# Kernel tuning notes

Hardware: AMD Instinct MI355X
Metric: run time of the kernel (lower is better)

## Reference

```python
import jax, jax.numpy as jnp
import numpy as np

N = 50000
E = 800000
NUM_GRAPHS = 64

def gat_layer(x, W, att_src, att_dst, bias, src, dst, heads, out_ch, concat):
    n = x.shape[0]
    h = (x @ W).reshape(n, heads, out_ch)                      # [N,H,C]
    a_s = jnp.sum(h * att_src, axis=-1)                        # [N,H]
    a_d = jnp.sum(h * att_dst, axis=-1)                        # [N,H]
    e = jax.nn.leaky_relu(a_s[src] + a_d[dst], 0.2)            # [E,H]
    m = jax.ops.segment_max(e, dst, num_segments=n)            # segment softmax (self-loops guarantee non-empty)
    e = jnp.exp(e - m[dst])
    s = jax.ops.segment_sum(e, dst, num_segments=n)
    alpha = e / s[dst]                                         # [E,H]
    out = jax.ops.segment_sum(alpha[:, :, None] * h[src], dst, num_segments=n)  # [N,H,C]
    out = out.reshape(n, heads * out_ch) if concat else out.mean(axis=1)
    return out + bias

def setup_inputs() -> dict:
    key = jax.random.key(0)
    ks = jax.random.split(key, 20)
    inp = {}
    inp['x'] = jax.random.normal(ks[0], (N, 256), dtype=jnp.float32)
    inp['edge_index'] = jax.random.randint(ks[1], (2, E), 0, N, dtype=jnp.int64)
    inp['batch'] = jnp.sort(jax.random.randint(ks[2], (N,), 0, NUM_GRAPHS, dtype=jnp.int64))
    s = 0.05
    inp['W1'] = jax.random.normal(ks[3], (256, 256), dtype=jnp.float32) * s
    inp['att_src1'] = jax.random.normal(ks[4], (8, 32), dtype=jnp.float32) * s
    inp['att_dst1'] = jax.random.normal(ks[5], (8, 32), dtype=jnp.float32) * s
    inp['b1'] = jax.random.normal(ks[6], (256,), dtype=jnp.float32) * s
    inp['W2'] = jax.random.normal(ks[7], (256, 256), dtype=jnp.float32) * s
    inp['att_src2'] = jax.random.normal(ks[8], (8, 32), dtype=jnp.float32) * s
    inp['att_dst2'] = jax.random.normal(ks[9], (8, 32), dtype=jnp.float32) * s
    inp['b2'] = jax.random.normal(ks[10], (256,), dtype=jnp.float32) * s
    inp['W3'] = jax.random.normal(ks[11], (256, 32), dtype=jnp.float32) * s
    inp['att_src3'] = jax.random.normal(ks[12], (1, 32), dtype=jnp.float32) * s
    inp['att_dst3'] = jax.random.normal(ks[13], (1, 32), dtype=jnp.float32) * s
    inp['b3'] = jax.random.normal(ks[14], (32,), dtype=jnp.float32) * s
    inp['linW'] = jax.random.normal(ks[15], (32, 1), dtype=jnp.float32) * s
    inp['linb'] = jax.random.normal(ks[16], (1,), dtype=jnp.float32) * s
    return inp

def reference(x, edge_index, batch, W1, att_src1, att_dst1, b1, W2, att_src2, att_dst2, b2,
              W3, att_src3, att_dst3, b3, linW, linb):
    # add self loops (PyG add_self_loops=True)
    loop = jnp.arange(N, dtype=edge_index.dtype)
    src = jnp.concatenate([edge_index[0], loop])
    dst = jnp.concatenate([edge_index[1], loop])
    # eval mode: dropout is identity
    h = gat_layer(x, W1, att_src1, att_dst1, b1, src, dst, 8, 32, True)
    h = jax.nn.elu(h)
    h = gat_layer(h, W2, att_src2, att_dst2, b2, src, dst, 8, 32, True)
    h = jax.nn.elu(h)
    h = gat_layer(h, W3, att_src3, att_dst3, b3, src, dst, 1, 32, False)
    # global mean pool over all nodes (topic_mask defaults to all True)
    sums = jax.ops.segment_sum(h, batch, num_segments=NUM_GRAPHS)
    cnts = jax.ops.segment_sum(jnp.ones((N,), h.dtype), batch, num_segments=NUM_GRAPHS)
    pooled = sums / jnp.maximum(cnts, 1.0)[:, None]
    out = pooled @ linW + linb                                  # [G,1]
    return out.squeeze(-1)                                      # num_classes==2
```

## Files before the change

kernel.cpp:

```cpp
#include <hip/hip_runtime.h>
#include <hip/hip_fp8.h>
#include <math.h>


typedef __attribute__((ext_vector_type(8))) __bf16 bf16x8;
typedef __attribute__((ext_vector_type(4))) __bf16 bf16x4;
typedef __attribute__((ext_vector_type(4))) float f32x4;
typedef __attribute__((ext_vector_type(2))) float f32x2;

#define SCAN_CH 4

__device__ inline unsigned char f32_to_fp8(float f) {
  __hip_fp8_e4m3 v(f);
  return (unsigned char)v.__x;
}
__device__ inline float fp8_to_f32(unsigned char u) {
  __hip_fp8_e4m3 v;
  v.__x = (__hip_fp8_storage_t)u;
  return (float)v;
}

__device__ inline void fma_fp8x4(f32x4& acc, float w, unsigned int packed) {
#if defined(__has_builtin) && __has_builtin(__builtin_amdgcn_cvt_pk_f32_fp8)
  f32x2 lo = __builtin_amdgcn_cvt_pk_f32_fp8((int)packed, false);
  f32x2 hi = __builtin_amdgcn_cvt_pk_f32_fp8((int)packed, true);
  acc[0] += w * lo[0];
  acc[1] += w * lo[1];
  acc[2] += w * hi[0];
  acc[3] += w * hi[1];
#else
  acc[0] += w * fp8_to_f32((unsigned char)(packed & 0xff));
  acc[1] += w * fp8_to_f32((unsigned char)((packed >> 8) & 0xff));
  acc[2] += w * fp8_to_f32((unsigned char)((packed >> 16) & 0xff));
  acc[3] += w * fp8_to_f32((unsigned char)(packed >> 24));
#endif
}

__global__ __launch_bounds__(256) void k_init_deg(int* deg, int N) {
  int n = blockIdx.x * 256 + threadIdx.x;
  if (n < N) deg[n] = 1;
}

__global__ __launch_bounds__(256) void k_count_deg(const int* __restrict__ ei,
                                                   int E, int* deg) {
  int e = blockIdx.x * 256 + threadIdx.x;
  if (e < E) atomicAdd(&deg[ei[E + e]], 1);
}

__global__ __launch_bounds__(256) void k_scan_partial(const int* __restrict__ deg,
                                                      int* __restrict__ blockSums,
                                                      int N) {
  __shared__ int sh[256];
  int t = threadIdx.x, b = blockIdx.x;
  int base = (b * 256 + t) * SCAN_CH;
  int s = 0;
#pragma unroll
  for (int j = 0; j < SCAN_CH; j++) {
    int idx = base + j;
    if (idx < N) s += deg[idx];
  }
  sh[t] = s;
  __syncthreads();
  for (int off = 128; off > 0; off >>= 1) {
    if (t < off) sh[t] += sh[t + off];
    __syncthreads();
  }
  if (t == 0) blockSums[b] = sh[0];
}

__global__ __launch_bounds__(256) void k_scan_blocksums(
    const int* __restrict__ blockSums, int* __restrict__ blockOffs,
    int* __restrict__ rowptr, int nb, int N) {
  __shared__ int sh[256];
  int t = threadIdx.x;
  int v = (t < nb) ? blockSums[t] : 0;
  sh[t] = v;
  __syncthreads();
  for (int off = 1; off < 256; off <<= 1) {
    int u = (t >= off) ? sh[t - off] : 0;
    __syncthreads();
    sh[t] += u;
    __syncthreads();
  }
  if (t < nb) blockOffs[t] = sh[t] - v;
  if (t == nb - 1) rowptr[N] = sh[t];
}

__global__ __launch_bounds__(256) void k_scan_final(const int* __restrict__ deg,
                                                    const int* __restrict__ blockOffs,
                                                    int* __restrict__ rowptr,
                                                    int* __restrict__ cursor, int N) {
  __shared__ int sh[256];
  int t = threadIdx.x, b = blockIdx.x;
  int base = (b * 256 + t) * SCAN_CH;
  int vals[SCAN_CH];
  int s = 0;
#pragma unroll
  for (int j = 0; j < SCAN_CH; j++) {
    int idx = base + j;
    vals[j] = (idx < N) ? deg[idx] : 0;
    s += vals[j];
  }
  sh[t] = s;
  __syncthreads();
  for (int off = 1; off < 256; off <<= 1) {
    int u = (t >= off) ? sh[t - off] : 0;
    __syncthreads();
    sh[t] += u;
    __syncthreads();
  }
  int run = blockOffs[b] + sh[t] - s;
#pragma unroll
  for (int j = 0; j < SCAN_CH; j++) {
    int idx = base + j;
    if (idx < N) {
      rowptr[idx] = run;
      cursor[idx] = run;
      run += vals[j];
    }
  }
}

__global__ __launch_bounds__(256) void k_scatter2(const int* __restrict__ ei,
                                                  int E, int N, int* cursor,
                                                  int2* __restrict__ col2,
                                                  int chunkSz) {
  int stripe = blockIdx.x & 7;
  int chunk = blockIdx.x >> 3;
  int lo = (int)(((long long)N * stripe) >> 3);
  int hi = (int)(((long long)N * (stripe + 1)) >> 3);
  int base = chunk * chunkSz;
  int end = base + chunkSz;
  int total = E + N;
  if (end > total) end = total;
  for (int i = base + threadIdx.x; i < end; i += 256) {
    int d = (i < E) ? ei[E + i] : (i - E);
    if (d < lo || d >= hi) continue;
    int s = (i < E) ? ei[i] : d;
    int pos = atomicAdd(&cursor[d], 1);
    col2[pos] = make_int2(s, d);
  }
}

__global__ __launch_bounds__(256) void k_split(const float* __restrict__ in,
                                               __bf16* __restrict__ oh,
                                               __bf16* __restrict__ ol, int n4) {
  int i = blockIdx.x * 256 + threadIdx.x;
  if (i >= n4) return;
  float4 v = ((const float4*)in)[i];
  bf16x4 h, l;
  h[0] = (__bf16)v.x; l[0] = (__bf16)(v.x - (float)h[0]);
  h[1] = (__bf16)v.y; l[1] = (__bf16)(v.y - (float)h[1]);
  h[2] = (__bf16)v.z; l[2] = (__bf16)(v.z - (float)h[2]);
  h[3] = (__bf16)v.w; l[3] = (__bf16)(v.w - (float)h[3]);
  ((bf16x4*)oh)[i] = h;
  ((bf16x4*)ol)[i] = l;
}

__global__ __launch_bounds__(256) void k_wprep(const float* __restrict__ W,
                                               __bf16* __restrict__ WTh,
                                               int K, int Nc) {
  int i = blockIdx.x * 256 + threadIdx.x;
  if (i >= K * Nc) return;
  int n = i / K, k = i - n * K;
  WTh[i] = (__bf16)W[k * Nc + n];
}

__global__ __launch_bounds__(256) void k_gemm_lds(
    const __bf16* __restrict__ Ah, const __bf16* __restrict__ Al,
    const __bf16* __restrict__ BTh,
    __bf16* __restrict__ Ch, unsigned char* __restrict__ Cf8, int M, int K) {
  constexpr int NcFull = 256;
  __shared__ __bf16 sAh[2][2048];
  __shared__ __bf16 sAl[2][2048];
  int tid = threadIdx.x;
  int lane = tid & 63, wave = tid >> 6;
  int quad = lane >> 4, l16 = lane & 15;
  int m0 = blockIdx.x * 64;
  int col0 = wave * 64;
  int sr = tid >> 2, skq = tid & 3;
  int slot8 = (((sr >> 4) * 4 + skq) * 16 + (sr & 15)) * 8;
  int arow = min(m0 + sr, M - 1);
  const __bf16* agh = Ah + (size_t)arow * K + skq * 8;
  const __bf16* agl = Al + (size_t)arow * K + skq * 8;
  const __bf16* brh = BTh + (size_t)(col0 + l16) * K + quad * 8;
  f32x4 acc[4][4];
#pragma unroll
  for (int mt = 0; mt < 4; mt++)
#pragma unroll
    for (int t = 0; t < 4; t++) acc[mt][t] = (f32x4){0.f, 0.f, 0.f, 0.f};
  *(bf16x8*)(sAh[0] + slot8) = *(const bf16x8*)agh;
  *(bf16x8*)(sAl[0] + slot8) = *(const bf16x8*)agl;
  __syncthreads();
  int buf = 0;
  for (int k0 = 0; k0 < K; k0 += 32, buf ^= 1) {
    bool more = (k0 + 32 < K);
    bf16x8 gh, gl;
    if (more) {
      gh = *(const bf16x8*)(agh + k0 + 32);
      gl = *(const bf16x8*)(agl + k0 + 32);
    }
    bf16x8 b_h[4];
#pragma unroll
    for (int t = 0; t < 4; t++)
      b_h[t] = *(const bf16x8*)(brh + (size_t)t * 16 * K + k0);
    const __bf16* rh = sAh[buf];
    const __bf16* rl = sAl[buf];
    bf16x8 a_h[4], a_l[4];
#pragma unroll
    for (int mt = 0; mt < 4; mt++) {
      int fi = ((mt * 4 + quad) * 16 + l16) * 8;
      a_h[mt] = *(const bf16x8*)(rh + fi);
      a_l[mt] = *(const bf16x8*)(rl + fi);
    }
#pragma unroll
    for (int t = 0; t < 4; t++) {
#pragma unroll
      for (int mt = 0; mt < 4; mt++) {
        acc[mt][t] = __builtin_amdgcn_mfma_f32_16x16x32_bf16(a_h[mt], b_h[t], acc[mt][t], 0, 0, 0);
        acc[mt][t] = __builtin_amdgcn_mfma_f32_16x16x32_bf16(a_l[mt], b_h[t], acc[mt][t], 0, 0, 0);
      }
    }
    if (more) {
      *(bf16x8*)(sAh[buf ^ 1] + slot8) = gh;
      *(bf16x8*)(sAl[buf ^ 1] + slot8) = gl;
    }
    __syncthreads();
  }
#pragma unroll
  for (int mt = 0; mt < 4; mt++) {
#pragma unroll
    for (int t = 0; t < 4; t++) {
#pragma unroll
      for (int r = 0; r < 4; r++) {
        int m = m0 + mt * 16 + quad * 4 + r;
        if (m < M) {
          size_t o = (size_t)m * NcFull + col0 + t * 16 + l16;
          Ch[o] = (__bf16)acc[mt][t][r];
          Cf8[o] = f32_to_fp8(acc[mt][t][r]);
        }
      }
    }
  }
}

template <int NT, int MT>
__global__ __launch_bounds__(256) void k_gemm_split(
    const __bf16* __restrict__ Ah, const __bf16* __restrict__ Al,
    const __bf16* __restrict__ BTh,
    __bf16* __restrict__ Ch, int M, int K, int NcFull) {
  int lane = threadIdx.x & 63;
  int wave = threadIdx.x >> 6;
  int quad = lane >> 4;
  int l16 = lane & 15;
  int m0 = blockIdx.y * (64 * MT) + wave * (16 * MT);
  int col0 = blockIdx.x * (NT * 16);
  const __bf16* arh[MT];
  const __bf16* arl[MT];
#pragma unroll
  for (int mt = 0; mt < MT; mt++) {
    int am = min(m0 + mt * 16 + l16, M - 1);
    arh[mt] = Ah + (size_t)am * K + quad * 8;
    arl[mt] = Al + (size_t)am * K + quad * 8;
  }
  const __bf16* brh = BTh + (size_t)(col0 + l16) * K + quad * 8;
  f32x4 acc[MT][NT];
#pragma unroll
  for (int mt = 0; mt < MT; mt++)
#pragma unroll
    for (int t = 0; t < NT; t++) acc[mt][t] = (f32x4){0.f, 0.f, 0.f, 0.f};
  for (int k0 = 0; k0 < K; k0 += 32) {
    bf16x8 a_h[MT], a_l[MT], b_h[NT];
#pragma unroll
    for (int mt = 0; mt < MT; mt++) {
      a_h[mt] = *(const bf16x8*)(arh[mt] + k0);
      a_l[mt] = *(const bf16x8*)(arl[mt] + k0);
    }
#pragma unroll
    for (int t = 0; t < NT; t++)
      b_h[t] = *(const bf16x8*)(brh + (size_t)t * 16 * K + k0);
#pragma unroll
    for (int t = 0; t < NT; t++) {
#pragma unroll
      for (int mt = 0; mt < MT; mt++) {
        acc[mt][t] = __builtin_amdgcn_mfma_f32_16x16x32_bf16(a_h[mt], b_h[t], acc[mt][t], 0, 0, 0);
        acc[mt][t] = __builtin_amdgcn_mfma_f32_16x16x32_bf16(a_l[mt], b_h[t], acc[mt][t], 0, 0, 0);
      }
    }
  }
#pragma unroll
  for (int mt = 0; mt < MT; mt++) {
#pragma unroll
    for (int t = 0; t < NT; t++) {
#pragma unroll
      for (int r = 0; r < 4; r++) {
        int m = m0 + mt * 16 + quad * 4 + r;
        if (m < M)
          Ch[(size_t)m * NcFull + col0 + t * 16 + l16] = (__bf16)acc[mt][t][r];
      }
    }
  }
}

__global__ __launch_bounds__(256) void k_att(const __bf16* __restrict__ Hh,
                                             const float* __restrict__ attS,
                                             const float* __restrict__ attD,
                                             float* __restrict__ aS,
                                             float* __restrict__ aD, int NH, int H) {
  int idx = blockIdx.x * 256 + threadIdx.x;
  if (idx >= NH) return;
  int h = idx % H;
  const bf16x8* hv = (const bf16x8*)(Hh + (size_t)idx * 32);
  const float* sv = attS + h * 32;
  const float* dv = attD + h * 32;
  float ss = 0.f, dd = 0.f;
#pragma unroll
  for (int k = 0; k < 4; k++) {
    bf16x8 a = hv[k];
#pragma unroll
    for (int j = 0; j < 8; j++) {
      float v = (float)a[j];
      ss += v * sv[k * 8 + j];
      dd += v * dv[k * 8 + j];
    }
  }
  aS[idx] = ss;
  aD[idx] = dd;
}

__global__ __launch_bounds__(256) void k_edge_alpha8(
    const float* __restrict__ aS, const float* __restrict__ aD,
    const int2* __restrict__ col2,
    __bf16* __restrict__ ealpha, int M) {
  int e = blockIdx.x * 256 + threadIdx.x;
  if (e >= M) return;
  int2 sd = col2[e];
  const float* ap = aS + (size_t)sd.x * 8;
  const float* dp = aD + (size_t)sd.y * 8;
  bf16x8 ev;
#pragma unroll
  for (int h = 0; h < 8; h++) {
    float x = ap[h] + dp[h];
    x = (x > 0.f) ? x : 0.2f * x;
    ev[h] = (__bf16)__expf(x);
  }
  *(bf16x8*)(ealpha + (size_t)e * 8) = ev;
}

__global__ __launch_bounds__(256) void k_edge_alpha1(
    const float* __restrict__ aS, const float* __restrict__ aD,
    const int2* __restrict__ col2,
    __bf16* __restrict__ ealpha, int M) {
  int e = blockIdx.x * 256 + threadIdx.x;
  if (e >= M) return;
  int2 sd = col2[e];
  float x = aS[sd.x] + aD[sd.y];
  x = (x > 0.f) ? x : 0.2f * x;
  ealpha[e] = (__bf16)__expf(x);
}

__global__ __launch_bounds__(256) void k_gat_agg8(
    const unsigned char* __restrict__ Hf8, const int* __restrict__ rowptr,
    const int2* __restrict__ col2, const __bf16* __restrict__ ealpha,
    const float* __restrict__ bias, __bf16* __restrict__ outh,
    __bf16* __restrict__ outl, int N) {
  int wid = (blockIdx.x * blockDim.x + threadIdx.x) >> 6;
  int lane = threadIdx.x & 63;
  if (wid >= N) return;
  int n = wid;
  int row0 = rowptr[n];
  int deg = rowptr[n + 1] - row0;
  int head = lane >> 3;

  f32x4 acc = (f32x4){0.f, 0.f, 0.f, 0.f};
  float den = 0.f;
  const __bf16* ea = ealpha;
  int i = 0;
  for (; i + 3 < deg; i += 4) {
    int sl = row0 + i;
    int s0 = col2[sl + 0].x;
    int s1 = col2[sl + 1].x;
    int s2 = col2[sl + 2].x;
    int s3 = col2[sl + 3].x;
    float w0 = (float)ea[(size_t)(sl + 0) * 8 + head];
    float w1 = (float)ea[(size_t)(sl + 1) * 8 + head];
    float w2 = (float)ea[(size_t)(sl + 2) * 8 + head];
    float w3 = (float)ea[(size_t)(sl + 3) * 8 + head];
    unsigned int p0 = *(const unsigned int*)(Hf8 + (size_t)s0 * 256 + lane * 4);
    unsigned int p1 = *(const unsigned int*)(Hf8 + (size_t)s1 * 256 + lane * 4);
    unsigned int p2 = *(const unsigned int*)(Hf8 + (size_t)s2 * 256 + lane * 4);
    unsigned int p3 = *(const unsigned int*)(Hf8 + (size_t)s3 * 256 + lane * 4);
    den += w0 + w1 + w2 + w3;
    fma_fp8x4(acc, w0, p0);
    fma_fp8x4(acc, w1, p1);
    fma_fp8x4(acc, w2, p2);
    fma_fp8x4(acc, w3, p3);
  }
  for (; i < deg; i++) {
    int sl = row0 + i;
    int s0 = col2[sl].x;
    float w0 = (float)ea[(size_t)sl * 8 + head];
    unsigned int p0 = *(const unsigned int*)(Hf8 + (size_t)s0 * 256 + lane * 4);
    den += w0;
    fma_fp8x4(acc, w0, p0);
  }
  float rsv = 1.f / den;
  float4 bv = *(const float4*)(bias + lane * 4);
  bf16x4 hb, lb;
#pragma unroll
  for (int j = 0; j < 4; j++) {
    float v = acc[j] * rsv + ((const float*)&bv)[j];
    v = (v > 0.f) ? v : (__expf(v) - 1.f);
    hb[j] = (__bf16)v;
    lb[j] = (__bf16)(v - (float)hb[j]);
  }
  *(bf16x4*)(outh + (size_t)n * 256 + lane * 4) = hb;
  *(bf16x4*)(outl + (size_t)n * 256 + lane * 4) = lb;
}

__global__ __launch_bounds__(256) void k_gat_agg1(
    const __bf16* __restrict__ Hh, const int* __restrict__ rowptr,
    const int2* __restrict__ col2, const __bf16* __restrict__ ealpha,
    const float* __restrict__ bias, float* __restrict__ out, int N) {
  int wid = (blockIdx.x * blockDim.x + threadIdx.x) >> 6;
  int lane = threadIdx.x & 63;
  if (wid >= N) return;
  int n = wid;
  int row0 = rowptr[n];
  int deg = rowptr[n + 1] - row0;
  int eo = lane >> 3;
  int cl = lane & 7;
  f32x4 acc = (f32x4){0.f, 0.f, 0.f, 0.f};
  float den = 0.f;
  for (int i = eo; i < deg; i += 8) {
    int slot = row0 + i;
    int src = col2[slot].x;
    float w = (float)ealpha[slot];
    den += w;
    bf16x4 hv = *(const bf16x4*)(Hh + (size_t)src * 32 + cl * 4);
#pragma unroll
    for (int j = 0; j < 4; j++) acc[j] += w * (float)hv[j];
  }
#pragma unroll
  for (int off = 8; off < 64; off <<= 1) {
#pragma unroll
    for (int j = 0; j < 4; j++) acc[j] += __shfl_xor(acc[j], off, 64);
    den += __shfl_xor(den, off, 64);
  }
  if (eo == 0) {
    float rsv = 1.f / den;
#pragma unroll
    for (int j = 0; j < 4; j++)
      out[(size_t)n * 32 + cl * 4 + j] = acc[j] * rsv + bias[cl * 4 + j];
  }
}

__global__ __launch_bounds__(256) void k_pool_final(
    const float* __restrict__ h, const int* __restrict__ batch,
    const float* __restrict__ linW, const float* __restrict__ linb,
    float* __restrict__ out, int N) {
  __shared__ float sh[256];
  int g = blockIdx.x;
  int tid = threadIdx.x;
  int grp = tid >> 5, c = tid & 31;
  int lo = 0, hi = N;
  while (lo < hi) { int mid = (lo + hi) >> 1; if (batch[mid] < g) lo = mid + 1; else hi = mid; }
  int start = lo;
  hi = N;
  while (lo < hi) { int mid = (lo + hi) >> 1; if (batch[mid] < g + 1) lo = mid + 1; else hi = mid; }
  int end = lo;
  float acc = 0.f;
  for (int n = start + grp; n < end; n += 8) acc += h[(size_t)n * 32 + c];
  sh[tid] = acc;
  __syncthreads();
  if (tid < 32) {
    float s = 0.f;
#pragma unroll
    for (int j = 0; j < 8; j++) s += sh[j * 32 + tid];
    float v = s * linW[tid];
#pragma unroll
    for (int off = 16; off > 0; off >>= 1) v += __shfl_xor(v, off, 64);
    if (tid == 0) {
      float cnt = (float)(end - start);
      out[g] = v / fmaxf(cnt, 1.f) + linb[0];
    }
  }
}

extern "C" void kernel_launch(void* const* d_in, const int* in_sizes, int n_in,
                              void* d_out, int out_size, void* d_ws, size_t ws_size,
                              hipStream_t stream) {
  const float* x = (const float*)d_in[0];
  const int* ei = (const int*)d_in[1];
  const int* batch = (const int*)d_in[2];
  const float* W1 = (const float*)d_in[3];
  const float* as1 = (const float*)d_in[4];
  const float* ad1 = (const float*)d_in[5];
  const float* b1 = (const float*)d_in[6];
  const float* W2 = (const float*)d_in[7];
  const float* as2 = (const float*)d_in[8];
  const float* ad2 = (const float*)d_in[9];
  const float* b2 = (const float*)d_in[10];
  const float* W3 = (const float*)d_in[11];
  const float* as3 = (const float*)d_in[12];
  const float* ad3 = (const float*)d_in[13];
  const float* b3 = (const float*)d_in[14];
  const float* linW = (const float*)d_in[15];
  const float* linb = (const float*)d_in[16];

  const int N = in_sizes[0] / 256;
  const int E = in_sizes[1] / 2;
  const int NUM_GRAPHS = 64;
  float* out = (float*)d_out;

  char* ws = (char*)d_ws;
  size_t off = 0;
  auto alloc = [&](size_t bytes) -> void* {
    void* p = ws + off;
    off += (bytes + 255) & ~(size_t)255;
    return p;
  };
  __bf16* Hh = (__bf16*)alloc((size_t)N * 256 * 2);
  unsigned char* Hf8 = (unsigned char*)alloc((size_t)N * 256);
  __bf16* Ah = (__bf16*)alloc((size_t)N * 256 * 2);
  __bf16* Al = (__bf16*)alloc((size_t)N * 256 * 2);
  __bf16* ealpha = (__bf16*)alloc((size_t)(E + N) * 8 * 2);
  float* aS = (float*)alloc((size_t)N * 8 * 4);
  float* aD = (float*)alloc((size_t)N * 8 * 4);
  int* deg = (int*)alloc((size_t)N * 4);
  int* rowptr = (int*)alloc((size_t)(N + 1) * 4);
  int* cursor = (int*)alloc((size_t)(N + 1) * 4);
  int2* col2 = (int2*)alloc((size_t)(E + N) * 8);
  int* blockSums = (int*)alloc(256 * 4);
  int* blockOffs = (int*)alloc(256 * 4);
  __bf16* WT1h = (__bf16*)alloc(256 * 256 * 2);
  __bf16* WT2h = (__bf16*)alloc(256 * 256 * 2);
  __bf16* WT3h = (__bf16*)alloc(32 * 256 * 2);
  float* h3agg = (float*)Ah;

  k_split<<<(N * 64 + 255) / 256, 256, 0, stream>>>(x, Ah, Al, N * 64);
  k_wprep<<<(256 * 256 + 255) / 256, 256, 0, stream>>>(W1, WT1h, 256, 256);
  k_wprep<<<(256 * 256 + 255) / 256, 256, 0, stream>>>(W2, WT2h, 256, 256);
  k_wprep<<<(256 * 32 + 255) / 256, 256, 0, stream>>>(W3, WT3h, 256, 32);
  k_init_deg<<<(N + 255) / 256, 256, 0, stream>>>(deg, N);
  k_count_deg<<<(E + 255) / 256, 256, 0, stream>>>(ei, E, deg);
  const int nb = (N + 256 * SCAN_CH - 1) / (256 * SCAN_CH);
  k_scan_partial<<<nb, 256, 0, stream>>>(deg, blockSums, N);
  k_scan_blocksums<<<1, 256, 0, stream>>>(blockSums, blockOffs, rowptr, nb, N);
  k_scan_final<<<nb, 256, 0, stream>>>(deg, blockOffs, rowptr, cursor, N);
  {
    const int totalItems = E + N;
    const int nch = 256;
    const int chunkSz = (totalItems + nch - 1) / nch;
    k_scatter2<<<8 * nch, 256, 0, stream>>>(ei, E, N, cursor, col2, chunkSz);
  }

  const int aggBlocks = (N + 3) / 4;
  const int gemmBlocks = (N + 63) / 64;
  const int M = E + N;
  const int edgeBlocks = (M + 255) / 256;
  dim3 g3(1, (N + 63) / 64);

  k_gemm_lds<<<gemmBlocks, 256, 0, stream>>>(Ah, Al, WT1h, Hh, Hf8, N, 256);
  k_att<<<(N * 8 + 255) / 256, 256, 0, stream>>>(Hh, as1, ad1, aS, aD, N * 8, 8);
  k_edge_alpha8<<<edgeBlocks, 256, 0, stream>>>(aS, aD, col2, ealpha, M);
  k_gat_agg8<<<aggBlocks, 256, 0, stream>>>(Hf8, rowptr, col2, ealpha, b1,
                                            Ah, Al, N);
  k_gemm_lds<<<gemmBlocks, 256, 0, stream>>>(Ah, Al, WT2h, Hh, Hf8, N, 256);
  k_att<<<(N * 8 + 255) / 256, 256, 0, stream>>>(Hh, as2, ad2, aS, aD, N * 8, 8);
  k_edge_alpha8<<<edgeBlocks, 256, 0, stream>>>(aS, aD, col2, ealpha, M);
  k_gat_agg8<<<aggBlocks, 256, 0, stream>>>(Hf8, rowptr, col2, ealpha, b2,
                                            Ah, Al, N);
  k_gemm_split<2, 1><<<g3, 256, 0, stream>>>(Ah, Al, WT3h, Hh, N, 256, 32);
  k_att<<<(N + 255) / 256, 256, 0, stream>>>(Hh, as3, ad3, aS, aD, N, 1);
  k_edge_alpha1<<<edgeBlocks, 256, 0, stream>>>(aS, aD, col2, ealpha, M);
  k_gat_agg1<<<aggBlocks, 256, 0, stream>>>(Hh, rowptr, col2, ealpha, b3,
                                            h3agg, N);
  k_pool_final<<<NUM_GRAPHS, 256, 0, stream>>>(h3agg, batch, linW, linb, out, N);
}
```

Before: 506.4 us.

## Partition fp8 features and edge weights into column quarters for cache-local aggregation

The GEMM now writes its fp8 output as four 64-column planes, one per wave column slice, and edge attention weights are stored as four planes of head pairs. The aggregation kernel launches separate blocks per quarter, interleaved so that all blocks working on a quarter touch a table a quarter the size, improving L2 hit rates on random neighbor gathers. Each wave handles four edges in parallel with a shuffle reduction at the end. A separate source-index array is added so the gathers read 4-byte indices instead of int2 pairs. The cost is extra index writes during the scatter and four times as many rowptr, index and weight reads across quarters.

```diff
diff --git a/kernel.cpp b/kernel.cpp
--- a/kernel.cpp
+++ b/kernel.cpp
@@ -5,6 +5,7 @@
 
 typedef __attribute__((ext_vector_type(8))) __bf16 bf16x8;
 typedef __attribute__((ext_vector_type(4))) __bf16 bf16x4;
+typedef __attribute__((ext_vector_type(2))) __bf16 bf16x2;
 typedef __attribute__((ext_vector_type(4))) float f32x4;
 typedef __attribute__((ext_vector_type(2))) float f32x2;
 
@@ -124,6 +125,7 @@
 __global__ __launch_bounds__(256) void k_scatter2(const int* __restrict__ ei,
                                                   int E, int N, int* cursor,
                                                   int2* __restrict__ col2,
+                                                  int* __restrict__ col_s,
                                                   int chunkSz) {
   int stripe = blockIdx.x & 7;
   int chunk = blockIdx.x >> 3;
@@ -139,6 +141,7 @@
     int s = (i < E) ? ei[i] : d;
     int pos = atomicAdd(&cursor[d], 1);
     col2[pos] = make_int2(s, d);
+    col_s[pos] = s;
   }
 }
 
@@ -235,9 +238,9 @@
       for (int r = 0; r < 4; r++) {
         int m = m0 + mt * 16 + quad * 4 + r;
         if (m < M) {
-          size_t o = (size_t)m * NcFull + col0 + t * 16 + l16;
-          Ch[o] = (__bf16)acc[mt][t][r];
-          Cf8[o] = f32_to_fp8(acc[mt][t][r]);
+          int colq = t * 16 + l16;
+          Ch[(size_t)m * NcFull + col0 + colq] = (__bf16)acc[mt][t][r];
+          Cf8[((size_t)wave * M + m) * 64 + colq] = f32_to_fp8(acc[mt][t][r]);
         }
       }
     }
@@ -331,20 +334,26 @@
 __global__ __launch_bounds__(256) void k_edge_alpha8(
     const float* __restrict__ aS, const float* __restrict__ aD,
     const int2* __restrict__ col2,
-    __bf16* __restrict__ ealpha, int M) {
+    __bf16* __restrict__ eaq, int M) {
   int e = blockIdx.x * 256 + threadIdx.x;
   if (e >= M) return;
   int2 sd = col2[e];
   const float* ap = aS + (size_t)sd.x * 8;
   const float* dp = aD + (size_t)sd.y * 8;
-  bf16x8 ev;
+  float ev[8];
 #pragma unroll
   for (int h = 0; h < 8; h++) {
     float x = ap[h] + dp[h];
     x = (x > 0.f) ? x : 0.2f * x;
-    ev[h] = (__bf16)__expf(x);
-  }
-  *(bf16x8*)(ealpha + (size_t)e * 8) = ev;
+    ev[h] = __expf(x);
+  }
+#pragma unroll
+  for (int q = 0; q < 4; q++) {
+    bf16x2 pr;
+    pr[0] = (__bf16)ev[2 * q];
+    pr[1] = (__bf16)ev[2 * q + 1];
+    *(bf16x2*)(eaq + ((size_t)q * M + e) * 2) = pr;
+  }
 }
 
 __global__ __launch_bounds__(256) void k_edge_alpha1(
@@ -359,68 +368,66 @@
   ealpha[e] = (__bf16)__expf(x);
 }
 
-__global__ __launch_bounds__(256) void k_gat_agg8(
-    const unsigned char* __restrict__ Hf8, const int* __restrict__ rowptr,
-    const int2* __restrict__ col2, const __bf16* __restrict__ ealpha,
+__global__ __launch_bounds__(256) void k_gat_agg8q(
+    const unsigned char* __restrict__ Hf8q, const int* __restrict__ rowptr,
+    const int* __restrict__ col_s, const __bf16* __restrict__ eaq,
     const float* __restrict__ bias, __bf16* __restrict__ outh,
-    __bf16* __restrict__ outl, int N) {
-  int wid = (blockIdx.x * blockDim.x + threadIdx.x) >> 6;
+    __bf16* __restrict__ outl, int N, int Mslots) {
+  int x = blockIdx.x & 7;
+  int q = x >> 1;
+  int chunk = (blockIdx.x >> 3) * 2 + (x & 1);
+  int wave = threadIdx.x >> 6;
+  int node = chunk * 4 + wave;
+  if (node >= N) return;
   int lane = threadIdx.x & 63;
-  if (wid >= N) return;
-  int n = wid;
-  int row0 = rowptr[n];
-  int deg = rowptr[n + 1] - row0;
-  int head = lane >> 3;
-
+  int g = lane >> 4;
+  int l = lane & 15;
+  int hh = l >> 3;
+  int row0 = rowptr[node];
+  int deg = rowptr[node + 1] - row0;
+  const unsigned char* tab = Hf8q + (size_t)q * ((size_t)N * 64);
+  const __bf16* ea = eaq + (size_t)q * ((size_t)Mslots * 2);
   f32x4 acc = (f32x4){0.f, 0.f, 0.f, 0.f};
   float den = 0.f;
-  const __bf16* ea = ealpha;
-  int i = 0;
-  for (; i + 3 < deg; i += 4) {
-    int sl = row0 + i;
-    int s0 = col2[sl + 0].x;
-    int s1 = col2[sl + 1].x;
-    int s2 = col2[sl + 2].x;
-    int s3 = col2[sl + 3].x;
-    float w0 = (float)ea[(size_t)(sl + 0) * 8 + head];
-    float w1 = (float)ea[(size_t)(sl + 1) * 8 + head];
-    float w2 = (float)ea[(size_t)(sl + 2) * 8 + head];
-    float w3 = (float)ea[(size_t)(sl + 3) * 8 + head];
-    unsigned int p0 = *(const unsigned int*)(Hf8 + (size_t)s0 * 256 + lane * 4);
-    unsigned int p1 = *(const unsigned int*)(Hf8 + (size_t)s1 * 256 + lane * 4);
-    unsigned int p2 = *(const unsigned int*)(Hf8 + (size_t)s2 * 256 + lane * 4);
-    unsigned int p3 = *(const unsigned int*)(Hf8 + (size_t)s3 * 256 + lane * 4);
-    den += w0 + w1 + w2 + w3;
+  for (int i = 0; i < deg; i += 8) {
+    int e0 = i + g, e1 = i + 4 + g;
+    int sl0 = row0 + min(e0, deg - 1);
+    int sl1 = row0 + min(e1, deg - 1);
+    int s0 = col_s[sl0];
+    int s1 = col_s[sl1];
+    float w0 = (e0 < deg) ? (float)ea[(size_t)sl0 * 2 + hh] : 0.f;
+    float w1 = (e1 < deg) ? (float)ea[(size_t)sl1 * 2 + hh] : 0.f;
+    unsigned int p0 = *(const unsigned int*)(tab + (size_t)s0 * 64 + l * 4);
+    unsigned int p1 = *(const unsigned int*)(tab + (size_t)s1 * 64 + l * 4);
+    den += w0 + w1;
     fma_fp8x4(acc, w0, p0);
     fma_fp8x4(acc, w1, p1);
-    fma_fp8x4(acc, w2, p2);
-    fma_fp8x4(acc, w3, p3);
-  }
-  for (; i < deg; i++) {
-    int sl = row0 + i;
-    int s0 = col2[sl].x;
-    float w0 = (float)ea[(size_t)sl * 8 + head];
-    unsigned int p0 = *(const unsigned int*)(Hf8 + (size_t)s0 * 256 + lane * 4);
-    den += w0;
-    fma_fp8x4(acc, w0, p0);
-  }
-  float rsv = 1.f / den;
-  float4 bv = *(const float4*)(bias + lane * 4);
-  bf16x4 hb, lb;
-#pragma unroll
-  for (int j = 0; j < 4; j++) {
-    float v = acc[j] * rsv + ((const float*)&bv)[j];
-    v = (v > 0.f) ? v : (__expf(v) - 1.f);
-    hb[j] = (__bf16)v;
-    lb[j] = (__bf16)(v - (float)hb[j]);
-  }
-  *(bf16x4*)(outh + (size_t)n * 256 + lane * 4) = hb;
-  *(bf16x4*)(outl + (size_t)n * 256 + lane * 4) = lb;
+  }
+#pragma unroll
+  for (int off = 16; off < 64; off <<= 1) {
+#pragma unroll
+    for (int j = 0; j < 4; j++) acc[j] += __shfl_xor(acc[j], off, 64);
+    den += __shfl_xor(den, off, 64);
+  }
+  if (g == 0) {
+    float rsv = 1.f / den;
+    float4 bv = *(const float4*)(bias + q * 64 + l * 4);
+    bf16x4 hb, lb;
+#pragma unroll
+    for (int j = 0; j < 4; j++) {
+      float v = acc[j] * rsv + ((const float*)&bv)[j];
+      v = (v > 0.f) ? v : (__expf(v) - 1.f);
+      hb[j] = (__bf16)v;
+      lb[j] = (__bf16)(v - (float)hb[j]);
+    }
+    *(bf16x4*)(outh + (size_t)node * 256 + q * 64 + l * 4) = hb;
+    *(bf16x4*)(outl + (size_t)node * 256 + q * 64 + l * 4) = lb;
+  }
 }
 
 __global__ __launch_bounds__(256) void k_gat_agg1(
     const __bf16* __restrict__ Hh, const int* __restrict__ rowptr,
-    const int2* __restrict__ col2, const __bf16* __restrict__ ealpha,
+    const int* __restrict__ col_s, const __bf16* __restrict__ ealpha,
     const float* __restrict__ bias, float* __restrict__ out, int N) {
   int wid = (blockIdx.x * blockDim.x + threadIdx.x) >> 6;
   int lane = threadIdx.x & 63;
@@ -434,7 +441,7 @@
   float den = 0.f;
   for (int i = eo; i < deg; i += 8) {
     int slot = row0 + i;
-    int src = col2[slot].x;
+    int src = col_s[slot];
     float w = (float)ealpha[slot];
     den += w;
     bf16x4 hv = *(const bf16x4*)(Hh + (size_t)src * 32 + cl * 4);
@@ -531,6 +538,7 @@
   int* rowptr = (int*)alloc((size_t)(N + 1) * 4);
   int* cursor = (int*)alloc((size_t)(N + 1) * 4);
   int2* col2 = (int2*)alloc((size_t)(E + N) * 8);
+  int* col_s = (int*)alloc((size_t)(E + N) * 4);
   int* blockSums = (int*)alloc(256 * 4);
   int* blockOffs = (int*)alloc(256 * 4);
   __bf16* WT1h = (__bf16*)alloc(256 * 256 * 2);
@@ -552,10 +560,12 @@
     const int totalItems = E + N;
     const int nch = 256;
     const int chunkSz = (totalItems + nch - 1) / nch;
-    k_scatter2<<<8 * nch, 256, 0, stream>>>(ei, E, N, cursor, col2, chunkSz);
+    k_scatter2<<<8 * nch, 256, 0, stream>>>(ei, E, N, cursor, col2, col_s, chunkSz);
   }
 
   const int aggBlocks = (N + 3) / 4;
+  const int nodeChunks = (N + 3) / 4;
+  const int agg8qGrid = 8 * ((nodeChunks + 1) / 2);
   const int gemmBlocks = (N + 63) / 64;
   const int M = E + N;
   const int edgeBlocks = (M + 255) / 256;
@@ -564,17 +574,17 @@
   k_gemm_lds<<<gemmBlocks, 256, 0, stream>>>(Ah, Al, WT1h, Hh, Hf8, N, 256);
   k_att<<<(N * 8 + 255) / 256, 256, 0, stream>>>(Hh, as1, ad1, aS, aD, N * 8, 8);
   k_edge_alpha8<<<edgeBlocks, 256, 0, stream>>>(aS, aD, col2, ealpha, M);
-  k_gat_agg8<<<aggBlocks, 256, 0, stream>>>(Hf8, rowptr, col2, ealpha, b1,
-                                            Ah, Al, N);
+  k_gat_agg8q<<<agg8qGrid, 256, 0, stream>>>(Hf8, rowptr, col_s, ealpha, b1,
+                                             Ah, Al, N, M);
   k_gemm_lds<<<gemmBlocks, 256, 0, stream>>>(Ah, Al, WT2h, Hh, Hf8, N, 256);
   k_att<<<(N * 8 + 255) / 256, 256, 0, stream>>>(Hh, as2, ad2, aS, aD, N * 8, 8);
   k_edge_alpha8<<<edgeBlocks, 256, 0, stream>>>(aS, aD, col2, ealpha, M);
-  k_gat_agg8<<<aggBlocks, 256, 0, stream>>>(Hf8, rowptr, col2, ealpha, b2,
-                                            Ah, Al, N);
+  k_gat_agg8q<<<agg8qGrid, 256, 0, stream>>>(Hf8, rowptr, col_s, ealpha, b2,
+                                             Ah, Al, N, M);
   k_gemm_split<2, 1><<<g3, 256, 0, stream>>>(Ah, Al, WT3h, Hh, N, 256, 32);
   k_att<<<(N + 255) / 256, 256, 0, stream>>>(Hh, as3, ad3, aS, aD, N, 1);
   k_edge_alpha1<<<edgeBlocks, 256, 0, stream>>>(aS, aD, col2, ealpha, M);
-  k_gat_agg1<<<aggBlocks, 256, 0, stream>>>(Hh, rowptr, col2, ealpha, b3,
+  k_gat_agg1<<<aggBlocks, 256, 0, stream>>>(Hh, rowptr, col_s, ealpha, b3,
                                             h3agg, N);
   k_pool_final<<<NUM_GRAPHS, 256, 0, stream>>>(h3agg, batch, linW, linb, out, N);
 }
```

Result: slower. 616.7 us (+21.8%).

## Drop bf16 hi/lo split of activations and use packed source index array

Applied to the files above, without the earlier changes.

Activations are no longer split into high and low bf16 halves, so every GEMM runs a single MFMA per tile instead of two, and the split/low-part stores and loads are removed. The scatter also writes a separate dense int array of source indices, which the aggregation kernels read instead of strided int2 pairs. The cost is lower GEMM input precision (plain bf16 activations), which could push results past the tolerance, plus one extra index array written during CSR build.

```diff
diff --git a/kernel.cpp b/kernel.cpp
--- a/kernel.cpp
+++ b/kernel.cpp
@@ -124,6 +124,7 @@
 __global__ __launch_bounds__(256) void k_scatter2(const int* __restrict__ ei,
                                                   int E, int N, int* cursor,
                                                   int2* __restrict__ col2,
+                                                  int* __restrict__ col_s,
                                                   int chunkSz) {
   int stripe = blockIdx.x & 7;
   int chunk = blockIdx.x >> 3;
@@ -139,22 +140,21 @@
     int s = (i < E) ? ei[i] : d;
     int pos = atomicAdd(&cursor[d], 1);
     col2[pos] = make_int2(s, d);
-  }
-}
-
-__global__ __launch_bounds__(256) void k_split(const float* __restrict__ in,
-                                               __bf16* __restrict__ oh,
-                                               __bf16* __restrict__ ol, int n4) {
+    col_s[pos] = s;
+  }
+}
+
+__global__ __launch_bounds__(256) void k_cast(const float* __restrict__ in,
+                                              __bf16* __restrict__ oh, int n4) {
   int i = blockIdx.x * 256 + threadIdx.x;
   if (i >= n4) return;
   float4 v = ((const float4*)in)[i];
-  bf16x4 h, l;
-  h[0] = (__bf16)v.x; l[0] = (__bf16)(v.x - (float)h[0]);
-  h[1] = (__bf16)v.y; l[1] = (__bf16)(v.y - (float)h[1]);
-  h[2] = (__bf16)v.z; l[2] = (__bf16)(v.z - (float)h[2]);
-  h[3] = (__bf16)v.w; l[3] = (__bf16)(v.w - (float)h[3]);
+  bf16x4 h;
+  h[0] = (__bf16)v.x;
+  h[1] = (__bf16)v.y;
+  h[2] = (__bf16)v.z;
+  h[3] = (__bf16)v.w;
   ((bf16x4*)oh)[i] = h;
-  ((bf16x4*)ol)[i] = l;
 }
 
 __global__ __launch_bounds__(256) void k_wprep(const float* __restrict__ W,
@@ -167,12 +167,10 @@
 }
 
 __global__ __launch_bounds__(256) void k_gemm_lds(
-    const __bf16* __restrict__ Ah, const __bf16* __restrict__ Al,
-    const __bf16* __restrict__ BTh,
+    const __bf16* __restrict__ Ah, const __bf16* __restrict__ BTh,
     __bf16* __restrict__ Ch, unsigned char* __restrict__ Cf8, int M, int K) {
   constexpr int NcFull = 256;
   __shared__ __bf16 sAh[2][2048];
-  __shared__ __bf16 sAl[2][2048];
   int tid = threadIdx.x;
   int lane = tid & 63, wave = tid >> 6;
   int quad = lane >> 4, l16 = lane & 15;
@@ -182,7 +180,6 @@
   int slot8 = (((sr >> 4) * 4 + skq) * 16 + (sr & 15)) * 8;
   int arow = min(m0 + sr, M - 1);
   const __bf16* agh = Ah + (size_t)arow * K + skq * 8;
-  const __bf16* agl = Al + (size_t)arow * K + skq * 8;
   const __bf16* brh = BTh + (size_t)(col0 + l16) * K + quad * 8;
   f32x4 acc[4][4];
 #pragma unroll
@@ -190,40 +187,34 @@
 #pragma unroll
     for (int t = 0; t < 4; t++) acc[mt][t] = (f32x4){0.f, 0.f, 0.f, 0.f};
   *(bf16x8*)(sAh[0] + slot8) = *(const bf16x8*)agh;
-  *(bf16x8*)(sAl[0] + slot8) = *(const bf16x8*)agl;
   __syncthreads();
   int buf = 0;
   for (int k0 = 0; k0 < K; k0 += 32, buf ^= 1) {
     bool more = (k0 + 32 < K);
-    bf16x8 gh, gl;
+    bf16x8 gh;
     if (more) {
       gh = *(const bf16x8*)(agh + k0 + 32);
-      gl = *(const bf16x8*)(agl + k0 + 32);
     }
     bf16x8 b_h[4];
 #pragma unroll
     for (int t = 0; t < 4; t++)
       b_h[t] = *(const bf16x8*)(brh + (size_t)t * 16 * K + k0);
     const __bf16* rh = sAh[buf];
-    const __bf16* rl = sAl[buf];
-    bf16x8 a_h[4], a_l[4];
+    bf16x8 a_h[4];
 #pragma unroll
     for (int mt = 0; mt < 4; mt++) {
       int fi = ((mt * 4 + quad) * 16 + l16) * 8;
       a_h[mt] = *(const bf16x8*)(rh + fi);
-      a_l[mt] = *(const bf16x8*)(rl + fi);
     }
 #pragma unroll
     for (int t = 0; t < 4; t++) {
 #pragma unroll
       for (int mt = 0; mt < 4; mt++) {
         acc[mt][t] = __builtin_amdgcn_mfma_f32_16x16x32_bf16(a_h[mt], b_h[t], acc[mt][t], 0, 0, 0);
-        acc[mt][t] = __builtin_amdgcn_mfma_f32_16x16x32_bf16(a_l[mt], b_h[t], acc[mt][t], 0, 0, 0);
       }
     }
     if (more) {
       *(bf16x8*)(sAh[buf ^ 1] + slot8) = gh;
-      *(bf16x8*)(sAl[buf ^ 1] + slot8) = gl;
     }
     __syncthreads();
   }
@@ -246,8 +237,7 @@
 
 template <int NT, int MT>
 __global__ __launch_bounds__(256) void k_gemm_split(
-    const __bf16* __restrict__ Ah, const __bf16* __restrict__ Al,
-    const __bf16* __restrict__ BTh,
+    const __bf16* __restrict__ Ah, const __bf16* __restrict__ BTh,
     __bf16* __restrict__ Ch, int M, int K, int NcFull) {
   int lane = threadIdx.x & 63;
   int wave = threadIdx.x >> 6;
@@ -256,12 +246,10 @@
   int m0 = blockIdx.y * (64 * MT) + wave * (16 * MT);
   int col0 = blockIdx.x * (NT * 16);
   const __bf16* arh[MT];
-  const __bf16* arl[MT];
 #pragma unroll
   for (int mt = 0; mt < MT; mt++) {
     int am = min(m0 + mt * 16 + l16, M - 1);
     arh[mt] = Ah + (size_t)am * K + quad * 8;
-    arl[mt] = Al + (size_t)am * K + quad * 8;
   }
   const __bf16* brh = BTh + (size_t)(col0 + l16) * K + quad * 8;
   f32x4 acc[MT][NT];
@@ -270,11 +258,10 @@
 #pragma unroll
     for (int t = 0; t < NT; t++) acc[mt][t] = (f32x4){0.f, 0.f, 0.f, 0.f};
   for (int k0 = 0; k0 < K; k0 += 32) {
-    bf16x8 a_h[MT], a_l[MT], b_h[NT];
+    bf16x8 a_h[MT], b_h[NT];
 #pragma unroll
     for (int mt = 0; mt < MT; mt++) {
       a_h[mt] = *(const bf16x8*)(arh[mt] + k0);
-      a_l[mt] = *(const bf16x8*)(arl[mt] + k0);
     }
 #pragma unroll
     for (int t = 0; t < NT; t++)
@@ -284,7 +271,6 @@
 #pragma unroll
       for (int mt = 0; mt < MT; mt++) {
         acc[mt][t] = __builtin_amdgcn_mfma_f32_16x16x32_bf16(a_h[mt], b_h[t], acc[mt][t], 0, 0, 0);
-        acc[mt][t] = __builtin_amdgcn_mfma_f32_16x16x32_bf16(a_l[mt], b_h[t], acc[mt][t], 0, 0, 0);
       }
     }
   }
@@ -361,9 +347,8 @@
 
 __global__ __launch_bounds__(256) void k_gat_agg8(
     const unsigned char* __restrict__ Hf8, const int* __restrict__ rowptr,
-    const int2* __restrict__ col2, const __bf16* __restrict__ ealpha,
-    const float* __restrict__ bias, __bf16* __restrict__ outh,
-    __bf16* __restrict__ outl, int N) {
+    const int* __restrict__ col_s, const __bf16* __restrict__ ealpha,
+    const float* __restrict__ bias, __bf16* __restrict__ outh, int N) {
   int wid = (blockIdx.x * blockDim.x + threadIdx.x) >> 6;
   int lane = threadIdx.x & 63;
   if (wid >= N) return;
@@ -378,10 +363,10 @@
   int i = 0;
   for (; i + 3 < deg; i += 4) {
     int sl = row0 + i;
-    int s0 = col2[sl + 0].x;
-    int s1 = col2[sl + 1].x;
-    int s2 = col2[sl + 2].x;
-    int s3 = col2[sl + 3].x;
+    int s0 = col_s[sl + 0];
+    int s1 = col_s[sl + 1];
+    int s2 = col_s[sl + 2];
+    int s3 = col_s[sl + 3];
     float w0 = (float)ea[(size_t)(sl + 0) * 8 + head];
     float w1 = (float)ea[(size_t)(sl + 1) * 8 + head];
     float w2 = (float)ea[(size_t)(sl + 2) * 8 + head];
@@ -398,7 +383,7 @@
   }
   for (; i < deg; i++) {
     int sl = row0 + i;
-    int s0 = col2[sl].x;
+    int s0 = col_s[sl];
     float w0 = (float)ea[(size_t)sl * 8 + head];
     unsigned int p0 = *(const unsigned int*)(Hf8 + (size_t)s0 * 256 + lane * 4);
     den += w0;
@@ -406,21 +391,19 @@
   }
   float rsv = 1.f / den;
   float4 bv = *(const float4*)(bias + lane * 4);
-  bf16x4 hb, lb;
+  bf16x4 hb;
 #pragma unroll
   for (int j = 0; j < 4; j++) {
     float v = acc[j] * rsv + ((const float*)&bv)[j];
     v = (v > 0.f) ? v : (__expf(v) - 1.f);
     hb[j] = (__bf16)v;
-    lb[j] = (__bf16)(v - (float)hb[j]);
   }
   *(bf16x4*)(outh + (size_t)n * 256 + lane * 4) = hb;
-  *(bf16x4*)(outl + (size_t)n * 256 + lane * 4) = lb;
 }
 
 __global__ __launch_bounds__(256) void k_gat_agg1(
     const __bf16* __restrict__ Hh, const int* __restrict__ rowptr,
-    const int2* __restrict__ col2, const __bf16* __restrict__ ealpha,
+    const int* __restrict__ col_s, const __bf16* __restrict__ ealpha,
     const float* __restrict__ bias, float* __restrict__ out, int N) {
   int wid = (blockIdx.x * blockDim.x + threadIdx.x) >> 6;
   int lane = threadIdx.x & 63;
@@ -434,7 +417,7 @@
   float den = 0.f;
   for (int i = eo; i < deg; i += 8) {
     int slot = row0 + i;
-    int src = col2[slot].x;
+    int src = col_s[slot];
     float w = (float)ealpha[slot];
     den += w;
     bf16x4 hv = *(const bf16x4*)(Hh + (size_t)src * 32 + cl * 4);
@@ -523,7 +506,6 @@
   __bf16* Hh = (__bf16*)alloc((size_t)N * 256 * 2);
   unsigned char* Hf8 = (unsigned char*)alloc((size_t)N * 256);
   __bf16* Ah = (__bf16*)alloc((size_t)N * 256 * 2);
-  __bf16* Al = (__bf16*)alloc((size_t)N * 256 * 2);
   __bf16* ealpha = (__bf16*)alloc((size_t)(E + N) * 8 * 2);
   float* aS = (float*)alloc((size_t)N * 8 * 4);
   float* aD = (float*)alloc((size_t)N * 8 * 4);
@@ -531,6 +513,7 @@
   int* rowptr = (int*)alloc((size_t)(N + 1) * 4);
   int* cursor = (int*)alloc((size_t)(N + 1) * 4);
   int2* col2 = (int2*)alloc((size_t)(E + N) * 8);
+  int* col_s = (int*)alloc((size_t)(E + N) * 4);
   int* blockSums = (int*)alloc(256 * 4);
   int* blockOffs = (int*)alloc(256 * 4);
   __bf16* WT1h = (__bf16*)alloc(256 * 256 * 2);
@@ -538,7 +521,7 @@
   __bf16* WT3h = (__bf16*)alloc(32 * 256 * 2);
   float* h3agg = (float*)Ah;
 
-  k_split<<<(N * 64 + 255) / 256, 256, 0, stream>>>(x, Ah, Al, N * 64);
+  k_cast<<<(N * 64 + 255) / 256, 256, 0, stream>>>(x, Ah, N * 64);
   k_wprep<<<(256 * 256 + 255) / 256, 256, 0, stream>>>(W1, WT1h, 256, 256);
   k_wprep<<<(256 * 256 + 255) / 256, 256, 0, stream>>>(W2, WT2h, 256, 256);
   k_wprep<<<(256 * 32 + 255) / 256, 256, 0, stream>>>(W3, WT3h, 256, 32);
@@ -552,7 +535,7 @@
     const int totalItems = E + N;
     const int nch = 256;
     const int chunkSz = (totalItems + nch - 1) / nch;
-    k_scatter2<<<8 * nch, 256, 0, stream>>>(ei, E, N, cursor, col2, chunkSz);
+    k_scatter2<<<8 * nch, 256, 0, stream>>>(ei, E, N, cursor, col2, col_s, chunkSz);
   }
 
   const int aggBlocks = (N + 3) / 4;
@@ -561,20 +544,20 @@
   const int edgeBlocks = (M + 255) / 256;
   dim3 g3(1, (N + 63) / 64);
 
-  k_gemm_lds<<<gemmBlocks, 256, 0, stream>>>(Ah, Al, WT1h, Hh, Hf8, N, 256);
+  k_gemm_lds<<<gemmBlocks, 256, 0, stream>>>(Ah, WT1h, Hh, Hf8, N, 256);
   k_att<<<(N * 8 + 255) / 256, 256, 0, stream>>>(Hh, as1, ad1, aS, aD, N * 8, 8);
   k_edge_alpha8<<<edgeBlocks, 256, 0, stream>>>(aS, aD, col2, ealpha, M);
-  k_gat_agg8<<<aggBlocks, 256, 0, stream>>>(Hf8, rowptr, col2, ealpha, b1,
-                                            Ah, Al, N);
-  k_gemm_lds<<<gemmBlocks, 256, 0, stream>>>(Ah, Al, WT2h, Hh, Hf8, N, 256);
+  k_gat_agg8<<<aggBlocks, 256, 0, stream>>>(Hf8, rowptr, col_s, ealpha, b1,
+                                            Ah, N);
+  k_gemm_lds<<<gemmBlocks, 256, 0, stream>>>(Ah, WT2h, Hh, Hf8, N, 256);
   k_att<<<(N * 8 + 255) / 256, 256, 0, stream>>>(Hh, as2, ad2, aS, aD, N * 8, 8);
   k_edge_alpha8<<<edgeBlocks, 256, 0, stream>>>(aS, aD, col2, ealpha, M);
-  k_gat_agg8<<<aggBlocks, 256, 0, stream>>>(Hf8, rowptr, col2, ealpha, b2,
-                                            Ah, Al, N);
-  k_gemm_split<2, 1><<<g3, 256, 0, stream>>>(Ah, Al, WT3h, Hh, N, 256, 32);
+  k_gat_agg8<<<aggBlocks, 256, 0, stream>>>(Hf8, rowptr, col_s, ealpha, b2,
+                                            Ah, N);
+  k_gemm_split<2, 1><<<g3, 256, 0, stream>>>(Ah, WT3h, Hh, N, 256, 32);
   k_att<<<(N + 255) / 256, 256, 0, stream>>>(Hh, as3, ad3, aS, aD, N, 1);
   k_edge_alpha1<<<edgeBlocks, 256, 0, stream>>>(aS, aD, col2, ealpha, M);
-  k_gat_agg1<<<aggBlocks, 256, 0, stream>>>(Hh, rowptr, col2, ealpha, b3,
+  k_gat_agg1<<<aggBlocks, 256, 0, stream>>>(Hh, rowptr, col_s, ealpha, b3,
                                             h3agg, N);
   k_pool_final<<<NUM_GRAPHS, 256, 0, stream>>>(h3agg, batch, linW, linb, out, N);
 }
```

Result: faster. 488.5 us (-3.5%).
